# Kernel tuning notes

Hardware: AMD Instinct MI355X
Metric: run time of the kernel (lower is better)

## Reference

```python
import jax, jax.numpy as jnp
import numpy as np

B = 4096      # graphs
N = 21        # nodes per graph (EEG electrodes)
CIN = 512
H1 = 1024
H2 = 1024
COUT = 512
R = 4         # SE reduction
RANK = 10     # nodevec rank
EPS = 1e-5
THRESH = 0.1


def setup_inputs() -> dict:
    key = jax.random.key(0)
    ks = jax.random.split(key, 16)
    p = lambda i, shape, s=0.02: (jax.random.normal(ks[i], shape, jnp.float32) * s)
    return {
        "x": jax.random.normal(ks[0], (B * N, CIN), jnp.float32),
        "batch": jnp.arange(B * N, dtype=jnp.int32) // N,
        "nodevec1": jax.random.normal(ks[1], (N, RANK), jnp.float32),
        "nodevec2": jax.random.normal(ks[2], (RANK, N), jnp.float32),
        "se_w1": p(3, (CIN, CIN // R), 0.05),
        "se_w2": p(4, (CIN // R, CIN), 0.05),
        "W1": p(5, (CIN, H1)), "b1": jnp.zeros((H1,), jnp.float32),
        "W2": p(6, (H1, H2)), "b2": jnp.zeros((H2,), jnp.float32),
        "W3": p(7, (H2, COUT)), "b3": jnp.zeros((COUT,), jnp.float32),
        "bn1_g": jnp.ones((H1,), jnp.float32), "bn1_b": jnp.zeros((H1,), jnp.float32),
        "bn2_g": jnp.ones((H2,), jnp.float32), "bn2_b": jnp.zeros((H2,), jnp.float32),
        "bn3_g": jnp.ones((COUT,), jnp.float32), "bn3_b": jnp.zeros((COUT,), jnp.float32),
        "rs1_w": p(8, (CIN, H1)), "rs1_b": jnp.zeros((H1,), jnp.float32),
        "fc_w": p(9, (COUT, 2 * COUT)), "fc_b": jnp.zeros((2 * COUT,), jnp.float32),
    }


def _batchnorm(h, g, b):
    # training-mode BN: biased batch stats over the node dimension
    m = h.mean(0)
    v = h.var(0)
    return (h - m) * jax.lax.rsqrt(v + EPS) * g + b


def _gcn(A, h, W, b):
    # GCNConv with precomputed normalized+thresholded weights:
    # out = A_block_diag @ (h @ W) + b, done densely per graph since A is 21x21
    hm = (h @ W).reshape(B, N, -1)                 # [B, N, Cout]
    agg = jnp.einsum('ij,bjc->bic', A, hm)         # message passing per graph
    return agg.reshape(B * N, -1) + b


def _forward(x, batch, nodevec1, nodevec2, se_w1, se_w2,
             W1, b1, W2, b2, W3, b3,
             bn1_g, bn1_b, bn2_g, bn2_b, bn3_g, bn3_b,
             rs1_w, rs1_b, fc_w, fc_b):
    # SE layer on [B, N, C]: channel-wise gating from node-mean features
    x3 = x.reshape(B, N, CIN)
    y = jax.nn.sigmoid(jax.nn.relu(x3.mean(1) @ se_w1) @ se_w2)   # [B, C]
    xg = (x3 * y[:, None, :]).reshape(B * N, CIN)
    # adaptive adjacency: sigmoid(nv1 @ nv2), symmetric normalize, threshold
    adp = jax.nn.sigmoid(nodevec1 @ nodevec2)                      # [N, N]
    at = adp + jnp.eye(N, dtype=adp.dtype)
    deg = at.sum(1)
    dinv = jnp.where(deg > 0, deg ** -0.5, 0.0)
    A = dinv[:, None] * at * dinv[None, :]
    A = jnp.where(A > THRESH, A, 0.0)
    # layer 1 (+ projected residual, BN, relu; dropout omitted = eval)
    h = _batchnorm(_gcn(A, xg, W1, b1), bn1_g, bn1_b) + (xg @ rs1_w + rs1_b)
    h = jax.nn.relu(h)
    # layer 2 (h1 == h2 -> identity residual)
    h = jax.nn.relu(_batchnorm(_gcn(A, h, W2, b2), bn2_g, bn2_b) + h)
    # layer 3
    h = _batchnorm(_gcn(A, h, W3, b3), bn3_g, bn3_b)
    # global mean pool by graph id
    ssum = jax.ops.segment_sum(h, batch, num_segments=B)
    cnt = jax.ops.segment_sum(jnp.ones((h.shape[0], 1), h.dtype), batch, num_segments=B)
    pooled = ssum / cnt
    return pooled @ fc_w + fc_b                                    # [B, 2*COUT]


def reference(x, batch, nodevec1, nodevec2, se_w1, se_w2,
              W1, b1, W2, b2, W3, b3,
              bn1_g, bn1_b, bn2_g, bn2_b, bn3_g, bn3_b,
              rs1_w, rs1_b, fc_w, fc_b):
    return _forward(x, batch, nodevec1, nodevec2, se_w1, se_w2,
                    W1, b1, W2, b2, W3, b3,
                    bn1_g, bn1_b, bn2_g, bn2_b, bn3_g, bn3_b,
                    rs1_w, rs1_b, fc_w, fc_b)
```

## Files before the change

### kernel.cpp

```cpp
#include <hip/hip_runtime.h>

typedef _Float16 f16;
typedef f16 f16x2 __attribute__((ext_vector_type(2)));
typedef f16 f16x8 __attribute__((ext_vector_type(8)));
typedef float f32x4 __attribute__((ext_vector_type(4)));
typedef const void __attribute__((address_space(1)))* gas1;
typedef void __attribute__((address_space(3)))* las3;

#define NB 4096
#define NN 21
#define MROWS (NB*NN)
#define CIN 512
#define H1C 1024
#define H2C 1024
#define COUTC 512

__global__ void k_adj(const float* __restrict__ nv1, const float* __restrict__ nv2,
                      float* __restrict__ Aout) {
  __shared__ float at[21][21];
  __shared__ float dinv[21];
  int t = threadIdx.x;
  if (t < 441) {
    int i = t / 21, j = t % 21;
    float s = 0.f;
    #pragma unroll
    for (int r = 0; r < 10; r++) s += nv1[i*10 + r] * nv2[r*21 + j];
    float v = 1.f / (1.f + expf(-s));
    if (i == j) v += 1.f;
    at[i][j] = v;
  }
  __syncthreads();
  if (t < 21) {
    float d = 0.f;
    #pragma unroll
    for (int j = 0; j < 21; j++) d += at[t][j];
    dinv[t] = d > 0.f ? rsqrtf(d) : 0.f;
  }
  __syncthreads();
  if (t < 441) {
    int i = t / 21, j = t % 21;
    float a = dinv[i] * at[i][j] * dinv[j];
    Aout[t] = a > 0.1f ? a : 0.f;
  }
}

__global__ void k_transpose(const float* __restrict__ src, f16* __restrict__ dst,
                            int K, int N) {
  __shared__ float tile[32][33];
  int n0 = blockIdx.x * 32, k0 = blockIdx.y * 32;
  int tx = threadIdx.x, ty = threadIdx.y;
  #pragma unroll
  for (int i = 0; i < 4; i++)
    tile[ty + 8*i][tx] = src[(size_t)(k0 + ty + 8*i) * N + n0 + tx];
  __syncthreads();
  #pragma unroll
  for (int i = 0; i < 4; i++)
    dst[(size_t)(n0 + ty + 8*i) * K + k0 + tx] = (f16)tile[tx][ty + 8*i];
}

__global__ void k_mean(const float* __restrict__ x, float* __restrict__ xm) {
  int b = blockIdx.x, t = threadIdx.x;
  for (int c = t; c < CIN; c += 256) {
    float s = 0.f;
    #pragma unroll
    for (int n = 0; n < NN; n++) s += x[((size_t)b*NN + n)*CIN + c];
    xm[(size_t)b*CIN + c] = s * (1.f/21.f);
  }
}

__global__ void k_se1(const float* __restrict__ xm, const float* __restrict__ w1,
                      float* __restrict__ y1) {
  __shared__ float row[CIN];
  int b = blockIdx.x, t = threadIdx.x;
  for (int k = t; k < CIN; k += 128) row[k] = xm[(size_t)b*CIN + k];
  __syncthreads();
  float acc = 0.f;
  for (int k = 0; k < CIN; k++) acc += row[k] * w1[(size_t)k*128 + t];
  y1[(size_t)b*128 + t] = fmaxf(acc, 0.f);
}

__global__ void k_se2(const float* __restrict__ y1, const float* __restrict__ w2,
                      float* __restrict__ y) {
  __shared__ float row[128];
  int b = blockIdx.x, t = threadIdx.x;
  if (t < 128) row[t] = y1[(size_t)b*128 + t];
  __syncthreads();
  float acc = 0.f;
  for (int k = 0; k < 128; k++) acc += row[k] * w2[(size_t)k*CIN + t];
  y[(size_t)b*CIN + t] = 1.f / (1.f + expf(-acc));
}

__global__ void k_gate(const float* __restrict__ x, const float* __restrict__ y,
                       f16* __restrict__ xg) {
  size_t i8 = (size_t)blockIdx.x * 256 + threadIdx.x;
  size_t base = i8 * 8;
  int r = (int)(base >> 9);
  int c = (int)(base & 511);
  int b = r / 21;
  const float4* xp = (const float4*)(x + base);
  const float4* yp = (const float4*)(y + (size_t)b*CIN + c);
  float4 a0 = xp[0], a1 = xp[1];
  float4 g0 = yp[0], g1 = yp[1];
  f16x8 o;
  o[0] = (f16)(a0.x * g0.x); o[1] = (f16)(a0.y * g0.y);
  o[2] = (f16)(a0.z * g0.z); o[3] = (f16)(a0.w * g0.w);
  o[4] = (f16)(a1.x * g1.x); o[5] = (f16)(a1.y * g1.y);
  o[6] = (f16)(a1.z * g1.z); o[7] = (f16)(a1.w * g1.w);
  *(f16x8*)(xg + base) = o;
}

#define GEMM_PRE(A_, BT_, K_, lgn_)                                            \
  __shared__ __align__(16) f16 As[128*32];                                     \
  __shared__ __align__(16) f16 Bs[128*32];                                     \
  const int tid = threadIdx.x;                                                 \
  const int nwg = gridDim.x;                                                   \
  const int g = blockIdx.x;                                                    \
  const int swz = (g & 7) * (nwg >> 3) + (g >> 3);                             \
  const int bn = swz & ((1 << (lgn_)) - 1);                                    \
  const int bm = swz >> (lgn_);                                                \
  const int lane = tid & 63;                                                   \
  const int wr = (tid >> 7) & 1;                                               \
  const int wc = (tid >> 6) & 1;                                               \
  const int srow = tid >> 2;                                                   \
  const int scol = (tid & 3) << 3;                                             \
  const f16* Ag = (A_) + (size_t)(bm*128 + srow) * (K_) + scol;                \
  const f16* Bg = (BT_) + (size_t)(bn*128 + srow) * (K_) + scol;               \
  f16* AsP = As + tid * 8;                                                     \
  f16* BsP = Bs + tid * 8;                                                     \
  const size_t rstep = (size_t)64 * (K_);                                      \
  const int fr = lane & 15;                                                    \
  const int kg = (lane >> 4) << 3;                                             \
  const f16* ArP = As + (wr*64 + fr)*32 + kg;                                  \
  const f16* BrP = Bs + (wc*64 + fr)*32 + kg;                                  \
  f32x4 acc[4][4];                                                             \
  _Pragma("unroll") for (int m = 0; m < 4; m++)                                \
    _Pragma("unroll") for (int n = 0; n < 4; n++)                              \
      _Pragma("unroll") for (int r = 0; r < 4; r++) acc[m][n][r] = 0.f;        \
  for (int kt = 0; kt < (K_); kt += 32) {                                      \
    __builtin_amdgcn_global_load_lds((gas1)(Ag + kt),         (las3)AsP,           16, 0, 0); \
    __builtin_amdgcn_global_load_lds((gas1)(Ag + kt + rstep), (las3)(AsP + 64*32), 16, 0, 0); \
    __builtin_amdgcn_global_load_lds((gas1)(Bg + kt),         (las3)BsP,           16, 0, 0); \
    __builtin_amdgcn_global_load_lds((gas1)(Bg + kt + rstep), (las3)(BsP + 64*32), 16, 0, 0); \
    __syncthreads();                                                           \
    f16x8 af[4], bv[4];                                                        \
    _Pragma("unroll") for (int m = 0; m < 4; m++) af[m] = *(const f16x8*)(ArP + m*16*32); \
    _Pragma("unroll") for (int n = 0; n < 4; n++) bv[n] = *(const f16x8*)(BrP + n*16*32); \
    _Pragma("unroll") for (int m = 0; m < 4; m++)                              \
      _Pragma("unroll") for (int n = 0; n < 4; n++)                            \
        acc[m][n] = __builtin_amdgcn_mfma_f32_16x16x32_f16(af[m], bv[n], acc[m][n], 0, 0, 0); \
    __syncthreads();                                                           \
  }                                                                            \
  const int crow = bm*128 + wr*64 + ((lane >> 4) << 2);                        \
  const int ccol0 = bn*128 + wc*64 + fr;

__global__ __launch_bounds__(256)
void k_gemm(const f16* __restrict__ A, const f16* __restrict__ BT,
            f16* __restrict__ C, int N, int K, int lgn) {
  GEMM_PRE(A, BT, K, lgn)
  #pragma unroll
  for (int m = 0; m < 4; m++)
    #pragma unroll
    for (int n = 0; n < 4; n++)
      #pragma unroll
      for (int r = 0; r < 4; r++)
        C[(size_t)(crow + m*16 + r) * N + (ccol0 + n*16)] = (f16)acc[m][n][r];
}

__global__ __launch_bounds__(256)
void k_gemm2(const f16* __restrict__ A, const f16* __restrict__ BT,
             f16* __restrict__ C1, f16* __restrict__ C2, int K) {
  GEMM_PRE(A, BT, K, 4)
  f16* Cp = C1; int cc = ccol0;
  if (ccol0 >= 1024) { Cp = C2; cc = ccol0 - 1024; }
  #pragma unroll
  for (int m = 0; m < 4; m++)
    #pragma unroll
    for (int n = 0; n < 4; n++)
      #pragma unroll
      for (int r = 0; r < 4; r++)
        Cp[(size_t)(crow + m*16 + r) * 1024 + (cc + n*16)] = (f16)acc[m][n][r];
}

__global__ __launch_bounds__(256)
void k_gemm_fc(const f16* __restrict__ A, const f16* __restrict__ BT,
               const float* __restrict__ bias, float* __restrict__ C,
               int N, int K, int lgn) {
  GEMM_PRE(A, BT, K, lgn)
  #pragma unroll
  for (int n = 0; n < 4; n++) {
    float bb = bias[ccol0 + n*16];
    #pragma unroll
    for (int m = 0; m < 4; m++)
      #pragma unroll
      for (int r = 0; r < 4; r++)
        C[(size_t)(crow + m*16 + r) * N + (ccol0 + n*16)] = acc[m][n][r] + bb;
  }
}

__global__ __launch_bounds__(256)
void k_mix(f16* __restrict__ t, const float* __restrict__ Aadj,
           float* __restrict__ psum, float* __restrict__ psq, int C) {
  __shared__ float A[441];
  int b = blockIdx.x, tid = threadIdx.x;
  for (int i = tid; i < 441; i += 256) A[i] = Aadj[i];
  __syncthreads();
  int c0 = (blockIdx.y * 256 + tid) * 2;
  size_t base = (size_t)b * NN * C + c0;
  float vx[21], vy[21];
  #pragma unroll
  for (int j = 0; j < 21; j++) {
    f16x2 v = *(const f16x2*)(t + base + (size_t)j * C);
    vx[j] = (float)v[0]; vy[j] = (float)v[1];
  }
  float s0 = 0.f, s1 = 0.f, q0 = 0.f, q1 = 0.f;
  #pragma unroll
  for (int i = 0; i < 21; i++) {
    float a0 = 0.f, a1 = 0.f;
    #pragma unroll
    for (int j = 0; j < 21; j++) {
      float w = A[i*21 + j];
      a0 = fmaf(w, vx[j], a0);
      a1 = fmaf(w, vy[j], a1);
    }
    f16x2 o; o[0] = (f16)a0; o[1] = (f16)a1;
    *(f16x2*)(t + base + (size_t)i * C) = o;
    s0 += a0; s1 += a1;
    q0 = fmaf(a0, a0, q0); q1 = fmaf(a1, a1, q1);
  }
  float2 sv; sv.x = s0; sv.y = s1;
  float2 qv; qv.x = q0; qv.y = q1;
  *(float2*)(psum + (size_t)b * C + c0) = sv;
  *(float2*)(psq  + (size_t)b * C + c0) = qv;
}

__global__ void k_reduce(const float* __restrict__ ps, const float* __restrict__ pq,
                         float* __restrict__ rs, float* __restrict__ rq, int C) {
  int c = blockIdx.x * 256 + threadIdx.x;
  int py = blockIdx.y;
  float s = 0.f, q = 0.f;
  for (int p = py*128; p < py*128 + 128; p++) {
    s += ps[(size_t)p*C + c];
    q += pq[(size_t)p*C + c];
  }
  rs[(size_t)py*C + c] = s;
  rq[(size_t)py*C + c] = q;
}

__global__ void k_bnparams(const float* __restrict__ psum, const float* __restrict__ psq,
                           const float* __restrict__ gamma, const float* __restrict__ beta,
                           const float* __restrict__ resbias,
                           float* __restrict__ scale, float* __restrict__ shift,
                           int C, int npart) {
  int c = blockIdx.x * 256 + threadIdx.x;
  float s = 0.f, q = 0.f;
  for (int p = 0; p < npart; p++) { s += psum[(size_t)p*C + c]; q += psq[(size_t)p*C + c]; }
  const float Minv = 1.f / (float)MROWS;
  float mean = s * Minv;
  float var = q * Minv - mean * mean;
  float sc = gamma[c] * rsqrtf(var + 1e-5f);
  float sh = beta[c] - mean * sc;
  if (resbias) sh += resbias[c];
  scale[c] = sc; shift[c] = sh;
}

__global__ void k_finalize(const f16* __restrict__ g, const f16* __restrict__ res,
                           f16* __restrict__ dst, const float* __restrict__ scale,
                           const float* __restrict__ shift, int cmask) {
  size_t i8 = (size_t)blockIdx.x * 256 + threadIdx.x;
  size_t base = i8 * 8;
  int c = (int)(base & (size_t)cmask);
  f16x8 gv = *(const f16x8*)(g + base);
  f16x8 rv = *(const f16x8*)(res + base);
  f16x8 o;
  #pragma unroll
  for (int j = 0; j < 8; j++) {
    float v = (float)gv[j] * scale[c + j] + shift[c + j] + (float)rv[j];
    o[j] = (f16)fmaxf(v, 0.f);
  }
  *(f16x8*)(dst + base) = o;
}

__global__ void k_pool(const f16* __restrict__ g3, const float* __restrict__ scale,
                       const float* __restrict__ shift, f16* __restrict__ pooled) {
  int b = blockIdx.x, t = threadIdx.x;
  for (int c = t; c < COUTC; c += 256) {
    float s = 0.f;
    #pragma unroll
    for (int n = 0; n < NN; n++) s += (float)g3[((size_t)b*NN + n)*COUTC + c];
    pooled[(size_t)b*COUTC + c] = (f16)((s * (1.f/21.f)) * scale[c] + shift[c]);
  }
}

extern "C" void kernel_launch(void* const* d_in, const int* in_sizes, int n_in,
                              void* d_out, int out_size, void* d_ws, size_t ws_size,
                              hipStream_t stream) {
  const float* x     = (const float*)d_in[0];
  const float* nv1   = (const float*)d_in[2];
  const float* nv2   = (const float*)d_in[3];
  const float* se_w1 = (const float*)d_in[4];
  const float* se_w2 = (const float*)d_in[5];
  const float* W1    = (const float*)d_in[6];
  const float* W2    = (const float*)d_in[8];
  const float* W3    = (const float*)d_in[10];
  const float* bn1g  = (const float*)d_in[12];
  const float* bn1b  = (const float*)d_in[13];
  const float* bn2g  = (const float*)d_in[14];
  const float* bn2b  = (const float*)d_in[15];
  const float* bn3g  = (const float*)d_in[16];
  const float* bn3b  = (const float*)d_in[17];
  const float* rs1w  = (const float*)d_in[18];
  const float* rs1b  = (const float*)d_in[19];
  const float* fcw   = (const float*)d_in[20];
  const float* fcb   = (const float*)d_in[21];
  float* out = (float*)d_out;

  char* ws = (char*)d_ws;
  size_t off = 0;
  auto alloc = [&](size_t bytes) -> char* {
    char* p = ws + off;
    off = (off + bytes + 255) & ~(size_t)255;
    return p;
  };

  float* A_adj = (float*)alloc(441 * 4);
  f16* W1R  = (f16*)alloc((size_t)2048 * CIN * 2);
  f16* W2T  = (f16*)alloc((size_t)H2C * H1C * 2);
  f16* W3T  = (f16*)alloc((size_t)COUTC * H2C * 2);
  f16* FCWT = (f16*)alloc((size_t)1024 * COUTC * 2);
  float* xm = (float*)alloc((size_t)NB * CIN * 4);
  float* y1 = (float*)alloc((size_t)NB * 128 * 4);
  float* yv = (float*)alloc((size_t)NB * CIN * 4);
  float* psum = (float*)alloc((size_t)NB * 1024 * 4);
  float* psq  = (float*)alloc((size_t)NB * 1024 * 4);
  float* rsum = (float*)alloc((size_t)32 * 1024 * 4);
  float* rsq  = (float*)alloc((size_t)32 * 1024 * 4);
  float* sc1 = (float*)alloc(1024 * 4);
  float* sh1 = (float*)alloc(1024 * 4);
  float* sc2 = (float*)alloc(1024 * 4);
  float* sh2 = (float*)alloc(1024 * 4);
  float* sc3 = (float*)alloc(1024 * 4);
  float* sh3 = (float*)alloc(1024 * 4);
  f16* pooled = (f16*)alloc((size_t)NB * COUTC * 2);
  f16* P1 = (f16*)alloc((size_t)MROWS * 512 * 2);
  f16* P2 = (f16*)alloc((size_t)MROWS * 1024 * 2);
  f16* P3 = (f16*)alloc((size_t)MROWS * 1024 * 2);
  (void)ws_size; (void)in_sizes; (void)n_in; (void)out_size;

  k_adj<<<1, 512, 0, stream>>>(nv1, nv2, A_adj);
  k_transpose<<<dim3(32, 16), dim3(32, 8), 0, stream>>>(W1,   W1R,                    512, 1024);
  k_transpose<<<dim3(32, 16), dim3(32, 8), 0, stream>>>(rs1w, W1R + (size_t)1024*512, 512, 1024);
  k_transpose<<<dim3(32, 32), dim3(32, 8), 0, stream>>>(W2,   W2T,  1024, 1024);
  k_transpose<<<dim3(16, 32), dim3(32, 8), 0, stream>>>(W3,   W3T,  1024, 512);
  k_transpose<<<dim3(32, 16), dim3(32, 8), 0, stream>>>(fcw,  FCWT, 512, 1024);

  k_mean<<<NB, 256, 0, stream>>>(x, xm);
  k_se1<<<NB, 128, 0, stream>>>(xm, se_w1, y1);
  k_se2<<<NB, 512, 0, stream>>>(y1, se_w2, yv);
  k_gate<<<21504, 256, 0, stream>>>(x, yv, P1);

  k_gemm2<<<672*16, 256, 0, stream>>>(P1, W1R, P2, P3, 512);
  k_mix<<<dim3(NB, 2), 256, 0, stream>>>(P2, A_adj, psum, psq, 1024);
  k_reduce<<<dim3(4, 32), 256, 0, stream>>>(psum, psq, rsum, rsq, 1024);
  k_bnparams<<<4, 256, 0, stream>>>(rsum, rsq, bn1g, bn1b, rs1b, sc1, sh1, 1024, 32);
  k_finalize<<<43008, 256, 0, stream>>>(P2, P3, P3, sc1, sh1, 1023);

  k_gemm<<<672*8, 256, 0, stream>>>(P3, W2T, P2, 1024, 1024, 3);
  k_mix<<<dim3(NB, 2), 256, 0, stream>>>(P2, A_adj, psum, psq, 1024);
  k_reduce<<<dim3(4, 32), 256, 0, stream>>>(psum, psq, rsum, rsq, 1024);
  k_bnparams<<<4, 256, 0, stream>>>(rsum, rsq, bn2g, bn2b, nullptr, sc2, sh2, 1024, 32);
  k_finalize<<<43008, 256, 0, stream>>>(P2, P3, P2, sc2, sh2, 1023);

  k_gemm<<<672*4, 256, 0, stream>>>(P2, W3T, P1, 512, 1024, 2);
  k_mix<<<dim3(NB, 1), 256, 0, stream>>>(P1, A_adj, psum, psq, 512);
  k_reduce<<<dim3(2, 32), 256, 0, stream>>>(psum, psq, rsum, rsq, 512);
  k_bnparams<<<2, 256, 0, stream>>>(rsum, rsq, bn3g, bn3b, nullptr, sc3, sh3, 512, 32);

  k_pool<<<NB, 256, 0, stream>>>(P1, sc3, sh3, pooled);
  k_gemm_fc<<<32*8, 256, 0, stream>>>(pooled, FCWT, fcb, out, 1024, COUTC, 3);
}
```

Measured before the change: 1.317 ms.

## Replace GEMMs with 128x256 triple-buffered, swizzled-LDS 8-wave MFMA kernel

Replaces the three 128x128 single-buffered GEMM kernels with one templated 512-thread kernel using 128x256 tiles, K-step 64, and a three-stage LDS ring fed by global_load_lds. LDS rows are XOR-swizzled to avoid bank conflicts, and loads for tile t+2 are issued between the two MFMA half-steps, with s_setprio raising priority during MFMA bursts. The aim is to hide global latency and raise arithmetic intensity in the dominant GEMMs. The cost is large LDS use (144KB, one block per CU) and fragile hand-written vmcnt/barrier synchronisation.

```diff
diff --git a/kernel.cpp b/kernel.cpp
--- a/kernel.cpp
+++ b/kernel.cpp
@@ -109,91 +109,159 @@
   *(f16x8*)(xg + base) = o;
 }
 
-#define GEMM_PRE(A_, BT_, K_, lgn_)                                            \
-  __shared__ __align__(16) f16 As[128*32];                                     \
-  __shared__ __align__(16) f16 Bs[128*32];                                     \
-  const int tid = threadIdx.x;                                                 \
-  const int nwg = gridDim.x;                                                   \
-  const int g = blockIdx.x;                                                    \
-  const int swz = (g & 7) * (nwg >> 3) + (g >> 3);                             \
-  const int bn = swz & ((1 << (lgn_)) - 1);                                    \
-  const int bm = swz >> (lgn_);                                                \
-  const int lane = tid & 63;                                                   \
-  const int wr = (tid >> 7) & 1;                                               \
-  const int wc = (tid >> 6) & 1;                                               \
-  const int srow = tid >> 2;                                                   \
-  const int scol = (tid & 3) << 3;                                             \
-  const f16* Ag = (A_) + (size_t)(bm*128 + srow) * (K_) + scol;                \
-  const f16* Bg = (BT_) + (size_t)(bn*128 + srow) * (K_) + scol;               \
-  f16* AsP = As + tid * 8;                                                     \
-  f16* BsP = Bs + tid * 8;                                                     \
-  const size_t rstep = (size_t)64 * (K_);                                      \
-  const int fr = lane & 15;                                                    \
-  const int kg = (lane >> 4) << 3;                                             \
-  const f16* ArP = As + (wr*64 + fr)*32 + kg;                                  \
-  const f16* BrP = Bs + (wc*64 + fr)*32 + kg;                                  \
-  f32x4 acc[4][4];                                                             \
-  _Pragma("unroll") for (int m = 0; m < 4; m++)                                \
-    _Pragma("unroll") for (int n = 0; n < 4; n++)                              \
-      _Pragma("unroll") for (int r = 0; r < 4; r++) acc[m][n][r] = 0.f;        \
-  for (int kt = 0; kt < (K_); kt += 32) {                                      \
-    __builtin_amdgcn_global_load_lds((gas1)(Ag + kt),         (las3)AsP,           16, 0, 0); \
-    __builtin_amdgcn_global_load_lds((gas1)(Ag + kt + rstep), (las3)(AsP + 64*32), 16, 0, 0); \
-    __builtin_amdgcn_global_load_lds((gas1)(Bg + kt),         (las3)BsP,           16, 0, 0); \
-    __builtin_amdgcn_global_load_lds((gas1)(Bg + kt + rstep), (las3)(BsP + 64*32), 16, 0, 0); \
-    __syncthreads();                                                           \
-    f16x8 af[4], bv[4];                                                        \
-    _Pragma("unroll") for (int m = 0; m < 4; m++) af[m] = *(const f16x8*)(ArP + m*16*32); \
-    _Pragma("unroll") for (int n = 0; n < 4; n++) bv[n] = *(const f16x8*)(BrP + n*16*32); \
-    _Pragma("unroll") for (int m = 0; m < 4; m++)                              \
-      _Pragma("unroll") for (int n = 0; n < 4; n++)                            \
-        acc[m][n] = __builtin_amdgcn_mfma_f32_16x16x32_f16(af[m], bv[n], acc[m][n], 0, 0, 0); \
-    __syncthreads();                                                           \
-  }                                                                            \
-  const int crow = bm*128 + wr*64 + ((lane >> 4) << 2);                        \
-  const int ccol0 = bn*128 + wc*64 + fr;
-
-__global__ __launch_bounds__(256)
-void k_gemm(const f16* __restrict__ A, const f16* __restrict__ BT,
-            f16* __restrict__ C, int N, int K, int lgn) {
-  GEMM_PRE(A, BT, K, lgn)
+#define GBM 128
+#define GBN 256
+#define BUFB 49152
+
+template<int MODE>
+__global__ __launch_bounds__(512, 1)
+void k_gemm8(const f16* __restrict__ A, const f16* __restrict__ BT,
+             f16* __restrict__ C1, f16* __restrict__ C2,
+             const float* __restrict__ bias, float* __restrict__ Cf,
+             int N, int K, int lgn) {
+  __shared__ __align__(16) char lds[3 * BUFB];
+  const int tid = threadIdx.x;
+  const int nwg = gridDim.x;
+  const int g = blockIdx.x;
+  const int swz = (g & 7) * (nwg >> 3) + (g >> 3);
+  const int bn = swz & ((1 << lgn) - 1);
+  const int bm = swz >> lgn;
+  const int lane = tid & 63;
+  const int wid = tid >> 6;
+  const int wr = wid >> 2;
+  const int wc = wid & 3;
+  const int fr = lane & 15;
+  const int kg = lane >> 4;
+
+  size_t srcOff[6]; int ldsOff[6];
+  #pragma unroll
+  for (int j = 0; j < 6; j++) {
+    int gid = j * 512 + tid;
+    if (gid < 1024) {
+      int row = gid >> 3, gr = gid & 7;
+      int gsw = gr ^ (row & 7);
+      srcOff[j] = (size_t)(bm * GBM + row) * K + gsw * 8;
+      ldsOff[j] = gid * 16;
+    } else {
+      int bgid = gid - 1024;
+      int row = bgid >> 3, gr = bgid & 7;
+      int gsw = gr ^ (row & 7);
+      srcOff[j] = (size_t)(bn * GBN + row) * K + gsw * 8;
+      ldsOff[j] = 16384 + bgid * 16;
+    }
+  }
+
+  int aOff[4], axor[4], bOff[4], bxor[4];
+  #pragma unroll
+  for (int m = 0; m < 4; m++) {
+    int row = wr*64 + m*16 + fr;
+    aOff[m] = row * 128; axor[m] = row & 7;
+  }
+  #pragma unroll
+  for (int n = 0; n < 4; n++) {
+    int row = wc*64 + n*16 + fr;
+    bOff[n] = 16384 + row * 128; bxor[n] = row & 7;
+  }
+
+  f32x4 acc[4][4];
   #pragma unroll
   for (int m = 0; m < 4; m++)
     #pragma unroll
     for (int n = 0; n < 4; n++)
       #pragma unroll
-      for (int r = 0; r < 4; r++)
-        C[(size_t)(crow + m*16 + r) * N + (ccol0 + n*16)] = (f16)acc[m][n][r];
-}
-
-__global__ __launch_bounds__(256)
-void k_gemm2(const f16* __restrict__ A, const f16* __restrict__ BT,
-             f16* __restrict__ C1, f16* __restrict__ C2, int K) {
-  GEMM_PRE(A, BT, K, 4)
-  f16* Cp = C1; int cc = ccol0;
-  if (ccol0 >= 1024) { Cp = C2; cc = ccol0 - 1024; }
-  #pragma unroll
-  for (int m = 0; m < 4; m++)
+      for (int r = 0; r < 4; r++) acc[m][n][r] = 0.f;
+
+  auto STAGE3 = [&](int t2, int sbuf, int j0) {
+    char* dst = (char*)lds + sbuf * BUFB;
+    const size_t kof = (size_t)t2 * 64;
+    #pragma unroll
+    for (int j = 0; j < 3; j++) {
+      int jj = j0 + j;
+      const f16* src = (jj < 2 ? A : BT) + srcOff[jj] + kof;
+      __builtin_amdgcn_global_load_lds((gas1)src, (las3)(dst + ldsOff[jj]), 16, 0, 0);
+    }
+  };
+
+  const int NT = K >> 6;
+  STAGE3(0, 0, 0); STAGE3(0, 0, 3);
+  STAGE3(1, 1, 0); STAGE3(1, 1, 3);
+  asm volatile("s_waitcnt vmcnt(6)" ::: "memory");
+  asm volatile("s_barrier" ::: "memory");
+
+  for (int t = 0; t < NT; t++) {
+    const int cb = t % 3;
+    const int sb = (t + 2) % 3;
+    const char* rb = (const char*)lds + cb * BUFB;
+    const bool ds = (t + 2) < NT;
+
+    f16x8 av[4], bv[4];
+    #pragma unroll
+    for (int m = 0; m < 4; m++)
+      av[m] = *(const f16x8*)(rb + aOff[m] + ((kg ^ axor[m]) << 4));
     #pragma unroll
     for (int n = 0; n < 4; n++)
-      #pragma unroll
-      for (int r = 0; r < 4; r++)
-        Cp[(size_t)(crow + m*16 + r) * 1024 + (cc + n*16)] = (f16)acc[m][n][r];
-}
-
-__global__ __launch_bounds__(256)
-void k_gemm_fc(const f16* __restrict__ A, const f16* __restrict__ BT,
-               const float* __restrict__ bias, float* __restrict__ C,
-               int N, int K, int lgn) {
-  GEMM_PRE(A, BT, K, lgn)
-  #pragma unroll
-  for (int n = 0; n < 4; n++) {
-    float bb = bias[ccol0 + n*16];
-    #pragma unroll
-    for (int m = 0; m < 4; m++)
-      #pragma unroll
-      for (int r = 0; r < 4; r++)
-        C[(size_t)(crow + m*16 + r) * N + (ccol0 + n*16)] = acc[m][n][r] + bb;
+      bv[n] = *(const f16x8*)(rb + bOff[n] + ((kg ^ bxor[n]) << 4));
+    if (ds) STAGE3(t + 2, sb, 0);
+    asm volatile("s_barrier" ::: "memory");
+    __builtin_amdgcn_s_setprio(1);
+    #pragma unroll
+    for (int m = 0; m < 4; m++)
+      #pragma unroll
+      for (int n = 0; n < 4; n++)
+        acc[m][n] = __builtin_amdgcn_mfma_f32_16x16x32_f16(av[m], bv[n], acc[m][n], 0, 0, 0);
+    __builtin_amdgcn_s_setprio(0);
+    asm volatile("s_barrier" ::: "memory");
+
+    #pragma unroll
+    for (int m = 0; m < 4; m++)
+      av[m] = *(const f16x8*)(rb + aOff[m] + (((4 + kg) ^ axor[m]) << 4));
+    #pragma unroll
+    for (int n = 0; n < 4; n++)
+      bv[n] = *(const f16x8*)(rb + bOff[n] + (((4 + kg) ^ bxor[n]) << 4));
+    if (ds) STAGE3(t + 2, sb, 3);
+    asm volatile("s_barrier" ::: "memory");
+    __builtin_amdgcn_s_setprio(1);
+    #pragma unroll
+    for (int m = 0; m < 4; m++)
+      #pragma unroll
+      for (int n = 0; n < 4; n++)
+        acc[m][n] = __builtin_amdgcn_mfma_f32_16x16x32_f16(av[m], bv[n], acc[m][n], 0, 0, 0);
+    __builtin_amdgcn_s_setprio(0);
+    if (ds) asm volatile("s_waitcnt vmcnt(6)" ::: "memory");
+    else    asm volatile("s_waitcnt vmcnt(0)" ::: "memory");
+    asm volatile("s_barrier" ::: "memory");
+  }
+
+  const int crow = bm * GBM + wr * 64 + ((lane >> 4) << 2);
+  const int ccol = bn * GBN + wc * 64 + fr;
+  if constexpr (MODE == 0) {
+    #pragma unroll
+    for (int m = 0; m < 4; m++)
+      #pragma unroll
+      for (int n = 0; n < 4; n++)
+        #pragma unroll
+        for (int r = 0; r < 4; r++)
+          C1[(size_t)(crow + m*16 + r) * N + (ccol + n*16)] = (f16)acc[m][n][r];
+  } else if constexpr (MODE == 1) {
+    f16* Cp = (bn < 4) ? C1 : C2;
+    const int cc = (bn & 3) * 256 + wc * 64 + fr;
+    #pragma unroll
+    for (int m = 0; m < 4; m++)
+      #pragma unroll
+      for (int n = 0; n < 4; n++)
+        #pragma unroll
+        for (int r = 0; r < 4; r++)
+          Cp[(size_t)(crow + m*16 + r) * 1024 + (cc + n*16)] = (f16)acc[m][n][r];
+  } else {
+    #pragma unroll
+    for (int n = 0; n < 4; n++) {
+      float bb = bias[ccol + n*16];
+      #pragma unroll
+      for (int m = 0; m < 4; m++)
+        #pragma unroll
+        for (int r = 0; r < 4; r++)
+          Cf[(size_t)(crow + m*16 + r) * N + (ccol + n*16)] = acc[m][n][r] + bb;
+    }
   }
 }
 
@@ -358,23 +426,23 @@
   k_se2<<<NB, 512, 0, stream>>>(y1, se_w2, yv);
   k_gate<<<21504, 256, 0, stream>>>(x, yv, P1);
 
-  k_gemm2<<<672*16, 256, 0, stream>>>(P1, W1R, P2, P3, 512);
+  k_gemm8<1><<<672*8, 512, 0, stream>>>(P1, W1R, P2, P3, nullptr, nullptr, 2048, 512, 3);
   k_mix<<<dim3(NB, 2), 256, 0, stream>>>(P2, A_adj, psum, psq, 1024);
   k_reduce<<<dim3(4, 32), 256, 0, stream>>>(psum, psq, rsum, rsq, 1024);
   k_bnparams<<<4, 256, 0, stream>>>(rsum, rsq, bn1g, bn1b, rs1b, sc1, sh1, 1024, 32);
   k_finalize<<<43008, 256, 0, stream>>>(P2, P3, P3, sc1, sh1, 1023);
 
-  k_gemm<<<672*8, 256, 0, stream>>>(P3, W2T, P2, 1024, 1024, 3);
+  k_gemm8<0><<<672*4, 512, 0, stream>>>(P3, W2T, P2, nullptr, nullptr, nullptr, 1024, 1024, 2);
   k_mix<<<dim3(NB, 2), 256, 0, stream>>>(P2, A_adj, psum, psq, 1024);
   k_reduce<<<dim3(4, 32), 256, 0, stream>>>(psum, psq, rsum, rsq, 1024);
   k_bnparams<<<4, 256, 0, stream>>>(rsum, rsq, bn2g, bn2b, nullptr, sc2, sh2, 1024, 32);
   k_finalize<<<43008, 256, 0, stream>>>(P2, P3, P2, sc2, sh2, 1023);
 
-  k_gemm<<<672*4, 256, 0, stream>>>(P2, W3T, P1, 512, 1024, 2);
+  k_gemm8<0><<<672*2, 512, 0, stream>>>(P2, W3T, P1, nullptr, nullptr, nullptr, 512, 1024, 1);
   k_mix<<<dim3(NB, 1), 256, 0, stream>>>(P1, A_adj, psum, psq, 512);
   k_reduce<<<dim3(2, 32), 256, 0, stream>>>(psum, psq, rsum, rsq, 512);
   k_bnparams<<<2, 256, 0, stream>>>(rsum, rsq, bn3g, bn3b, nullptr, sc3, sh3, 512, 32);
 
   k_pool<<<NB, 256, 0, stream>>>(P1, sc3, sh3, pooled);
-  k_gemm_fc<<<32*8, 256, 0, stream>>>(pooled, FCWT, fcb, out, 1024, COUTC, 3);
-}
+  k_gemm8<2><<<32*4, 512, 0, stream>>>(pooled, FCWT, nullptr, nullptr, fcb, out, 1024, 512, 2);
+}
```

New measurement: 1.215 ms. 1.08x faster.
